# Optimization experiments

Hardware: AMD Instinct MI355X
Metric: run time of the kernel (lower is better)

Reference implementation:

```python
import jax, jax.numpy as jnp
import numpy as np

N = 50000      # nodes
E = 400000     # edges (before self-loops)
IN = 128       # in_channels
OUT = 64       # out_channels (per-head; concat=False averages heads)
HEADS = 8      # heads of first GAT layer; second layer has 1 head
NEG_SLOPE = 0.2


def _glorot(key, shape, fan_in, fan_out):
    s = jnp.sqrt(2.0 / (fan_in + fan_out)).astype(jnp.float32)
    return jax.random.normal(key, shape, jnp.float32) * s


def setup_inputs() -> dict:
    key = jax.random.key(0)
    ks = jax.random.split(key, 10)
    x = jax.random.normal(ks[0], (N, IN), jnp.float32)
    edge_index = jax.random.randint(ks[1], (2, E), 0, N)
    # layer 1: heads=HEADS, per-head dim OUT
    W1 = _glorot(ks[2], (IN, HEADS * OUT), IN, HEADS * OUT)
    att_src1 = _glorot(ks[3], (HEADS, OUT), OUT, 1)
    att_dst1 = _glorot(ks[4], (HEADS, OUT), OUT, 1)
    b1 = jnp.zeros((OUT,), jnp.float32)
    # layer 2: heads=1
    W2 = _glorot(ks[5], (OUT, 1 * OUT), OUT, OUT)
    att_src2 = _glorot(ks[6], (1, OUT), OUT, 1)
    att_dst2 = _glorot(ks[7], (1, OUT), OUT, 1)
    b2 = jnp.zeros((OUT,), jnp.float32)
    return dict(x=x, edge_index=edge_index, W1=W1, att_src1=att_src1,
                att_dst1=att_dst1, b1=b1, W2=W2, att_src2=att_src2,
                att_dst2=att_dst2, b2=b2)


def gat_conv(x, edge_index, W, att_src, att_dst, bias, heads, ch):
    """PyG GATConv with concat=False (mean over heads), add_self_loops=True."""
    n = x.shape[0]
    loop = jnp.arange(n, dtype=edge_index.dtype)
    src = jnp.concatenate([edge_index[0], loop])  # [E+N]
    dst = jnp.concatenate([edge_index[1], loop])
    h = (x @ W).reshape(n, heads, ch)                     # [N, H, C]
    a_s = jnp.sum(h * att_src, axis=-1)                   # [N, H]
    a_d = jnp.sum(h * att_dst, axis=-1)                   # [N, H]
    e = jax.nn.leaky_relu(a_s[src] + a_d[dst], NEG_SLOPE)  # [E+N, H]
    # numerically stable segment softmax over incoming edges of each dst node
    emax = jax.lax.stop_gradient(
        jax.ops.segment_max(e, dst, num_segments=n))       # [N, H]
    ee = jnp.exp(e - emax[dst])
    denom = jax.ops.segment_sum(ee, dst, num_segments=n)  # [N, H]
    alpha = ee / denom[dst]                                # [E+N, H]
    out = jax.ops.segment_sum(alpha[:, :, None] * h[src], dst,
                              num_segments=n)              # [N, H, C]
    return out.mean(axis=1) + bias                         # [N, C]


def reference(x, edge_index, W1, att_src1, att_dst1, b1,
              W2, att_src2, att_dst2, b2):
    h = gat_conv(x, edge_index, W1, att_src1, att_dst1, b1, HEADS, OUT)
    h = jax.nn.elu(h)
    return gat_conv(h, edge_index, W2, att_src2, att_dst2, b2, 1, OUT)
```

## Files before the change

kernel.cpp:

```cpp
#include <hip/hip_runtime.h>
#include <cstdint>
#include <cstddef>

#define NEG_SLOPE 0.2f

typedef short bf16x8 __attribute__((ext_vector_type(8)));
typedef float f32x4 __attribute__((ext_vector_type(4)));
typedef float f32x2 __attribute__((ext_vector_type(2)));

__device__ __forceinline__ unsigned short f2bf(float f) {
  unsigned u = __float_as_uint(f);
  u = u + 0x7FFFu + ((u >> 16) & 1u);
  return (unsigned short)(u >> 16);
}
__device__ __forceinline__ float bf2f(unsigned short b) {
  return __uint_as_float((unsigned)b << 16);
}
__device__ __forceinline__ f32x2 unpk(unsigned xv) {
  f32x2 r;
  r.x = __uint_as_float(xv << 16);
  r.y = __uint_as_float(xv & 0xFFFF0000u);
  return r;
}
__device__ __forceinline__ float rlf(float v, int l) {
  return __uint_as_float(
      (unsigned)__builtin_amdgcn_readlane((int)__float_as_uint(v), l));
}

__global__ __launch_bounds__(256) void prep_all(
    const int* __restrict__ ei, int* __restrict__ counts,
    int* __restrict__ posb,
    const float* __restrict__ x, unsigned short* __restrict__ xb,
    const float* __restrict__ W1, const float* __restrict__ att_s1,
    const float* __restrict__ att_d1, unsigned short* __restrict__ AsAdT,
    unsigned short* __restrict__ WbT,
    const float* __restrict__ W2, unsigned short* __restrict__ W2t,
    const float* __restrict__ att_s2, const float* __restrict__ att_d2,
    float* __restrict__ AsAd2,
    int E, int ET, int N, int B0, int B1) {
  int b = blockIdx.x, tid = threadIdx.x;
  if (b < B0) {
    int i = b * 256 + tid;
    if (i < ET) {
      int dst = (i < E) ? ei[E + i] : (i - E);
      int pos = atomicAdd(&counts[dst], 1);
      posb[i] = pos;
    }
    return;
  }
  b -= B0;
  if (b < B1) {
    int i = b * 256 + tid;
    if (i < N * 32) {
      float4 v = ((const float4*)x)[i];
      ushort4 o;
      o.x = f2bf(v.x); o.y = f2bf(v.y); o.z = f2bf(v.z); o.w = f2bf(v.w);
      ((ushort4*)xb)[i] = o;
    }
    return;
  }
  b -= B1;
  if (b < 8) {
    int i = b * 256 + tid;
    int o = i >> 7, k = i & 127, h = o & 7;
    const float* att = (o < 8) ? att_s1 : att_d1;
    float s = 0.f;
    for (int c = 0; c < 64; c++) s += W1[(size_t)k * 512 + h * 64 + c] * att[h * 64 + c];
    AsAdT[i] = f2bf(s);
    return;
  }
  b -= 8;
  if (b < 256) {
    int i = b * 256 + tid;
    int o = i >> 10, k = i & 1023, h = k >> 7, c = k & 127;
    WbT[i] = f2bf(W1[(size_t)c * 512 + h * 64 + o]);
    return;
  }
  b -= 256;
  if (b < 16) {
    int i = b * 256 + tid;
    if (i < 64 * 64) {
      int k = i >> 6, nn = i & 63;
      W2t[(size_t)nn * 64 + k] = f2bf(W2[i]);
    }
    return;
  }
  {
    int i = tid;
    if (i < 128) {
      int o = i >> 6, k = i & 63;
      const float* att = (o == 0) ? att_s2 : att_d2;
      float s = 0.f;
      for (int c = 0; c < 64; c++) s += W2[(size_t)k * 64 + c] * att[c];
      AsAd2[i] = s;
    }
  }
}

__global__ __launch_bounds__(1024) void scan_dots(
    const int* __restrict__ counts, int* __restrict__ offsets,
    const unsigned short* __restrict__ xb, const unsigned short* __restrict__ AsAdT,
    float* __restrict__ asd, int n) {
  if (blockIdx.x == 0) {
    __shared__ int sums[1024];
    int t = threadIdx.x;
    int chunk = (n + 1023) >> 10;
    int start = t * chunk;
    int end = min(start + chunk, n);
    int s = 0;
    for (int i = start; i < end; i++) s += counts[i];
    sums[t] = s;
    __syncthreads();
    for (int off = 1; off < 1024; off <<= 1) {
      int v = (t >= off) ? sums[t - off] : 0;
      __syncthreads();
      sums[t] += v;
      __syncthreads();
    }
    int run = sums[t] - s;
    for (int i = start; i < end; i++) { offsets[i] = run; run += counts[i]; }
    if (t == 1023) offsets[n] = sums[1023];
    return;
  }
  int tid = threadIdx.x;
  int wave = tid >> 6, lane = tid & 63;
  int q = lane >> 4, t = lane & 15;
  int row0 = (blockIdx.x - 1) * 256 + wave * 16;
  int arow = row0 + t; if (arow > n - 1) arow = n - 1;
  const bf16x8* aptr = (const bf16x8*)(xb + (size_t)arow * 128);
  const bf16x8* bptr = (const bf16x8*)(AsAdT + t * 128);
  f32x4 acc = (f32x4){0.f, 0.f, 0.f, 0.f};
  #pragma unroll
  for (int s = 0; s < 4; s++)
    acc = __builtin_amdgcn_mfma_f32_16x16x32_bf16(aptr[s * 4 + q], bptr[s * 4 + q],
                                                  acc, 0, 0, 0);
  #pragma unroll
  for (int r = 0; r < 4; r++) {
    int row = row0 + q * 4 + r;
    if (row < n) asd[row * 16 + t] = acc[r];
  }
}

__global__ __launch_bounds__(256) void fill_csr(
    const int* __restrict__ ei, const int* __restrict__ offsets,
    const int* __restrict__ posb, int* __restrict__ srcs, int E, int ET) {
  int i = blockIdx.x * 256 + threadIdx.x;
  if (i >= ET) return;
  int src, dst;
  if (i < E) { src = ei[i]; dst = ei[E + i]; } else { src = dst = i - E; }
  srcs[offsets[dst] + posb[i]] = src;
}

#define CONSUME8R(RV, W, ACC)                                         \
  _Pragma("unroll")                                                   \
  for (int k = 0; k < 8; k++) {                                       \
    f32x2 x2 = unpk(RV[k]);                                           \
    ACC[0] += x2 * rlf(W, k * 8 + 0);                                 \
    ACC[1] += x2 * rlf(W, k * 8 + 1);                                 \
    ACC[2] += x2 * rlf(W, k * 8 + 2);                                 \
    ACC[3] += x2 * rlf(W, k * 8 + 3);                                 \
    ACC[4] += x2 * rlf(W, k * 8 + 4);                                 \
    ACC[5] += x2 * rlf(W, k * 8 + 5);                                 \
    ACC[6] += x2 * rlf(W, k * 8 + 6);                                 \
    ACC[7] += x2 * rlf(W, k * 8 + 7);                                 \
  }

__global__ __launch_bounds__(512, 8) void agg1_gemm(
    const int* __restrict__ offsets, const int* __restrict__ srcs,
    const float* __restrict__ asd, const unsigned short* __restrict__ xb,
    const unsigned short* __restrict__ WbT, const float* __restrict__ b1,
    const float* __restrict__ AsAd2, unsigned short* __restrict__ zb,
    float* __restrict__ as2, float* __restrict__ ad2, int N) {
  __shared__ unsigned short sh[8 * 1032];
  int tid = threadIdx.x;
  int wv = tid >> 6, lane = tid & 63;
  int nb = blockIdx.x;
  {
    int node = nb * 8 + wv;
    f32x2 acc[8];
    #pragma unroll
    for (int h = 0; h < 8; h++) acc[h] = (f32x2){0.f, 0.f};
    float wsl = 0.f;
    int beg = offsets[node], end = offsets[node + 1];
    int jl = end - 1;
    float adv = asd[(size_t)node * 16 + 8 + (lane & 7)];
    for (int cb = beg; cb < end; cb += 16) {
      int cnt = min(16, end - cb);
      int sAll = srcs[min(cb + (lane & 15), jl)];
      int swa = srcs[min(cb + (lane >> 3), jl)];
      float asva = asd[(size_t)(unsigned)swa * 16 + (lane & 7)];
      float asvb = 0.f;
      if (cnt > 8) {
        int swb = srcs[min(cb + 8 + (lane >> 3), jl)];
        asvb = asd[(size_t)(unsigned)swb * 16 + (lane & 7)];
      }
      unsigned rva[8] = {0, 0, 0, 0, 0, 0, 0, 0};
      unsigned rvb[8] = {0, 0, 0, 0, 0, 0, 0, 0};
      #pragma unroll
      for (int k = 0; k < 4; k++) {
        int se = __builtin_amdgcn_readlane(sAll, k);
        rva[k] = *(const unsigned*)&xb[(size_t)(unsigned)se * 128 + 2 * lane];
      }
      if (cnt > 4) {
        #pragma unroll
        for (int k = 4; k < 8; k++) {
          int se = __builtin_amdgcn_readlane(sAll, k);
          rva[k] = *(const unsigned*)&xb[(size_t)(unsigned)se * 128 + 2 * lane];
        }
      }
      if (cnt > 8) {
        #pragma unroll
        for (int k = 0; k < 4; k++) {
          int se = __builtin_amdgcn_readlane(sAll, k + 8);
          rvb[k] = *(const unsigned*)&xb[(size_t)(unsigned)se * 128 + 2 * lane];
        }
      }
      if (cnt > 12) {
        #pragma unroll
        for (int k = 4; k < 8; k++) {
          int se = __builtin_amdgcn_readlane(sAll, k + 8);
          rvb[k] = *(const unsigned*)&xb[(size_t)(unsigned)se * 128 + 2 * lane];
        }
      }
      float wa, wb = 0.f;
      {
        float v = asva + adv;
        v = (v > 0.f) ? v : NEG_SLOPE * v;
        wa = (cb + (lane >> 3) < end) ? __expf(v) : 0.f;
      }
      if (cnt > 8) {
        float v = asvb + adv;
        v = (v > 0.f) ? v : NEG_SLOPE * v;
        wb = (cb + 8 + (lane >> 3) < end) ? __expf(v) : 0.f;
      }
      wsl += wa + wb;
      CONSUME8R(rva, wa, acc);
      if (cnt > 8) { CONSUME8R(rvb, wb, acc); }
    }
    wsl += __shfl_xor(wsl, 8, 64);
    wsl += __shfl_xor(wsl, 16, 64);
    wsl += __shfl_xor(wsl, 32, 64);
    #pragma unroll
    for (int h = 0; h < 8; h++) {
      float tot = rlf(wsl, h);
      float iv = 0.125f / tot;
      unsigned o = (unsigned)f2bf(acc[h].x * iv) | ((unsigned)f2bf(acc[h].y * iv) << 16);
      *(unsigned*)&sh[wv * 1032 + h * 128 + 2 * lane] = o;
    }
  }
  __syncthreads();
  if (wv < 4) {
    int q = lane >> 4, t = lane & 15;
    f32x4 acc4 = (f32x4){0.f, 0.f, 0.f, 0.f};
    const unsigned short* bbase = WbT + (size_t)(wv * 16 + t) * 1024;
    #pragma unroll 8
    for (int s = 0; s < 32; s++) {
      bf16x8 af = *(const bf16x8*)&sh[(t & 7) * 1032 + s * 32 + q * 8];
      bf16x8 bf = *(const bf16x8*)&bbase[s * 32 + q * 8];
      acc4 = __builtin_amdgcn_mfma_f32_16x16x32_bf16(af, bf, acc4, 0, 0, 0);
    }
    int col = wv * 16 + t;
    float bias = b1[col];
    float vs = AsAd2[col], vd = AsAd2[64 + col];
    #pragma unroll
    for (int r = 0; r < 4; r++) {
      int row = q * 4 + r;
      float v = acc4[r] + bias;
      v = (v > 0.f) ? v : (__expf(v) - 1.f);
      float s = v * vs, d = v * vd;
      #pragma unroll
      for (int off = 1; off < 16; off <<= 1) {
        s += __shfl_xor(s, off, 64);
        d += __shfl_xor(d, off, 64);
      }
      if (row < 8) {
        int node = nb * 8 + row;
        zb[(size_t)node * 64 + col] = f2bf(v);
        if (t == 0) {
          atomicAdd(&as2[node], s);
          atomicAdd(&ad2[node], d);
        }
      }
    }
  }
}

__global__ __launch_bounds__(512, 8) void agg2_gemm(
    const int* __restrict__ offsets, const int* __restrict__ srcs,
    const float* __restrict__ as2, const float* __restrict__ ad2,
    const unsigned short* __restrict__ zb, const unsigned short* __restrict__ W2t,
    const float* __restrict__ b2, float* __restrict__ out, int N) {
  __shared__ unsigned short sh[8 * 72];
  int tid = threadIdx.x;
  int wv = tid >> 6, lane = tid & 63;
  int nb = blockIdx.x;
  {
    int node = nb * 8 + wv;
    int half = lane >> 5;
    float adv = ad2[node];
    int beg = offsets[node], end = offsets[node + 1];
    int jl = end - 1;
    f32x2 acc = (f32x2){0.f, 0.f};
    float wsl = 0.f;
    for (int cb = beg; cb < end; cb += 16) {
      int cnt = min(16, end - cb);
      int sAll = srcs[min(cb + (lane & 15), jl)];
      float asv = as2[sAll];
      unsigned rv[8] = {0, 0, 0, 0, 0, 0, 0, 0};
      #pragma unroll
      for (int k = 0; k < 2; k++) {
        int s0 = __builtin_amdgcn_readlane(sAll, 2 * k);
        int s1 = __builtin_amdgcn_readlane(sAll, 2 * k + 1);
        int se = half ? s1 : s0;
        rv[k] = *(const unsigned*)&zb[(size_t)(unsigned)se * 64 + 2 * (lane & 31)];
      }
      if (cnt > 4) {
        #pragma unroll
        for (int k = 2; k < 4; k++) {
          int s0 = __builtin_amdgcn_readlane(sAll, 2 * k);
          int s1 = __builtin_amdgcn_readlane(sAll, 2 * k + 1);
          int se = half ? s1 : s0;
          rv[k] = *(const unsigned*)&zb[(size_t)(unsigned)se * 64 + 2 * (lane & 31)];
        }
      }
      if (cnt > 8) {
        #pragma unroll
        for (int k = 4; k < 6; k++) {
          int s0 = __builtin_amdgcn_readlane(sAll, 2 * k);
          int s1 = __builtin_amdgcn_readlane(sAll, 2 * k + 1);
          int se = half ? s1 : s0;
          rv[k] = *(const unsigned*)&zb[(size_t)(unsigned)se * 64 + 2 * (lane & 31)];
        }
      }
      if (cnt > 12) {
        #pragma unroll
        for (int k = 6; k < 8; k++) {
          int s0 = __builtin_amdgcn_readlane(sAll, 2 * k);
          int s1 = __builtin_amdgcn_readlane(sAll, 2 * k + 1);
          int se = half ? s1 : s0;
          rv[k] = *(const unsigned*)&zb[(size_t)(unsigned)se * 64 + 2 * (lane & 31)];
        }
      }
      float v = asv + adv;
      v = (v > 0.f) ? v : NEG_SLOPE * v;
      float wl = (cb + (lane & 15) < end) ? __expf(v) : 0.f;
      if (lane < 16) wsl += wl;
      #pragma unroll
      for (int k = 0; k < 4; k++) {
        float w0 = rlf(wl, 2 * k);
        float w1 = rlf(wl, 2 * k + 1);
        float w = half ? w1 : w0;
        acc += unpk(rv[k]) * w;
      }
      if (cnt > 8) {
        #pragma unroll
        for (int k = 4; k < 8; k++) {
          float w0 = rlf(wl, 2 * k);
          float w1 = rlf(wl, 2 * k + 1);
          float w = half ? w1 : w0;
          acc += unpk(rv[k]) * w;
        }
      }
    }
    wsl += __shfl_xor(wsl, 1, 64);
    wsl += __shfl_xor(wsl, 2, 64);
    wsl += __shfl_xor(wsl, 4, 64);
    wsl += __shfl_xor(wsl, 8, 64);
    float tot = rlf(wsl, 0);
    acc.x += __shfl_xor(acc.x, 32, 64);
    acc.y += __shfl_xor(acc.y, 32, 64);
    if (lane < 32) {
      float inv = 1.f / tot;
      unsigned o = (unsigned)f2bf(acc.x * inv) | ((unsigned)f2bf(acc.y * inv) << 16);
      *(unsigned*)&sh[wv * 72 + 2 * lane] = o;
    }
  }
  __syncthreads();
  if (wv < 4) {
    int q = lane >> 4, t = lane & 15;
    f32x4 acc4 = (f32x4){0.f, 0.f, 0.f, 0.f};
    const unsigned short* bbase = W2t + (size_t)(wv * 16 + t) * 64;
    #pragma unroll
    for (int s = 0; s < 2; s++) {
      bf16x8 af = *(const bf16x8*)&sh[(t & 7) * 72 + s * 32 + q * 8];
      bf16x8 bf = *(const bf16x8*)&bbase[s * 32 + q * 8];
      acc4 = __builtin_amdgcn_mfma_f32_16x16x32_bf16(af, bf, acc4, 0, 0, 0);
    }
    int col = wv * 16 + t;
    float bias = b2[col];
    #pragma unroll
    for (int r = 0; r < 4; r++) {
      int row = q * 4 + r;
      if (row < 8) {
        int node = nb * 8 + row;
        if (node < N) out[(size_t)node * 64 + col] = acc4[r] + bias;
      }
    }
  }
}

extern "C" void kernel_launch(void* const* d_in, const int* in_sizes, int n_in,
                              void* d_out, int out_size, void* d_ws, size_t ws_size,
                              hipStream_t stream) {
  const int IN = 128;
  const int N = in_sizes[0] / IN;
  const int E = in_sizes[1] / 2;
  const int ET = E + N;

  const float* x        = (const float*)d_in[0];
  const int*   ei       = (const int*)d_in[1];
  const float* W1       = (const float*)d_in[2];
  const float* att_src1 = (const float*)d_in[3];
  const float* att_dst1 = (const float*)d_in[4];
  const float* b1       = (const float*)d_in[5];
  const float* W2       = (const float*)d_in[6];
  const float* att_src2 = (const float*)d_in[7];
  const float* att_dst2 = (const float*)d_in[8];
  const float* b2       = (const float*)d_in[9];
  float* out = (float*)d_out;

  char* base = (char*)d_ws;
  size_t off = 0;
  auto alloc = [&](size_t bytes) -> char* {
    char* p = base + off;
    off = (off + bytes + 255) & ~(size_t)255;
    return p;
  };
  unsigned short* xb    = (unsigned short*)alloc((size_t)N * 128 * 2);
  unsigned short* AsAdT = (unsigned short*)alloc((size_t)16 * 128 * 2);
  unsigned short* WbT   = (unsigned short*)alloc((size_t)64 * 1024 * 2);
  unsigned short* W2t   = (unsigned short*)alloc((size_t)64 * 64 * 2);
  unsigned short* zb    = (unsigned short*)alloc((size_t)N * 64 * 2);
  float* AsAd2 = (float*)alloc((size_t)128 * 4);
  float* asd1  = (float*)alloc((size_t)N * 16 * 4);
  int* offsets = (int*)alloc((size_t)(N + 1) * 4);
  int* srcs    = (int*)alloc((size_t)ET * 4);
  int* posb    = (int*)alloc((size_t)ET * 4);
  char* zero_begin = base + off;
  int* counts  = (int*)alloc((size_t)N * 4);
  float* a_s2  = (float*)alloc((size_t)N * 4);
  float* a_d2  = (float*)alloc((size_t)N * 4);
  char* zero_end = base + off;

  hipMemsetAsync(zero_begin, 0, (size_t)(zero_end - zero_begin), stream);

  const int TB = 256;
  auto cdiv = [](int a, int b) { return (a + b - 1) / b; };

  int B0 = cdiv(ET, TB);
  int B1 = cdiv(N * 32, TB);
  prep_all<<<B0 + B1 + 8 + 256 + 16 + 1, TB, 0, stream>>>(
      ei, counts, posb, x, xb, W1, att_src1, att_dst1, AsAdT, WbT, W2, W2t,
      att_src2, att_dst2, AsAd2, E, ET, N, B0, B1);

  scan_dots<<<1 + cdiv(N, 256), 1024, 0, stream>>>(counts, offsets, xb, AsAdT,
                                                   asd1, N);

  fill_csr<<<cdiv(ET, TB), TB, 0, stream>>>(ei, offsets, posb, srcs, E, ET);

  agg1_gemm<<<cdiv(N, 8), 512, 0, stream>>>(offsets, srcs, asd1, xb, WbT, b1,
                                            AsAd2, zb, a_s2, a_d2, N);

  agg2_gemm<<<cdiv(N, 8), 512, 0, stream>>>(offsets, srcs, a_s2, a_d2, zb,
                                            W2t, b2, out, N);
}
```

Before: 338.8 us.

## Process 16 nodes per block to fill MFMA rows and skip partial edge groups

Blocks of the two aggregation+GEMM kernels grow from 8 to 16 waves, so each handles 16 destination nodes. The MFMA tile's 16 rows are now all real nodes instead of half being duplicates, which halves the number of blocks and the per-node weight loads. The consume loops are also split into 4-edge chunks so partially filled 16-edge groups skip the unused multiply-adds. Larger 1024-thread blocks with a launch-bounds hint of 8 blocks per CU may squeeze register budgets or reduce occupancy flexibility, and the N<16-multiple boundary is no longer guarded in agg1.

```diff
diff --git a/kernel.cpp b/kernel.cpp
--- a/kernel.cpp
+++ b/kernel.cpp
@@ -151,32 +151,32 @@
   srcs[offsets[dst] + posb[i]] = src;
 }
 
-#define CONSUME8R(RV, W, ACC)                                         \
+#define CONSUME4R(RV, K0, W, ACC)                                     \
   _Pragma("unroll")                                                   \
-  for (int k = 0; k < 8; k++) {                                       \
+  for (int k = K0; k < K0 + 4; k++) {                                 \
     f32x2 x2 = unpk(RV[k]);                                           \
-    ACC[0] += x2 * rlf(W, k * 8 + 0);                                 \
-    ACC[1] += x2 * rlf(W, k * 8 + 1);                                 \
-    ACC[2] += x2 * rlf(W, k * 8 + 2);                                 \
-    ACC[3] += x2 * rlf(W, k * 8 + 3);                                 \
-    ACC[4] += x2 * rlf(W, k * 8 + 4);                                 \
-    ACC[5] += x2 * rlf(W, k * 8 + 5);                                 \
-    ACC[6] += x2 * rlf(W, k * 8 + 6);                                 \
-    ACC[7] += x2 * rlf(W, k * 8 + 7);                                 \
-  }
-
-__global__ __launch_bounds__(512, 8) void agg1_gemm(
+    ACC[0] += x2 * rlf(W, (k & 7) * 8 + 0);                           \
+    ACC[1] += x2 * rlf(W, (k & 7) * 8 + 1);                           \
+    ACC[2] += x2 * rlf(W, (k & 7) * 8 + 2);                           \
+    ACC[3] += x2 * rlf(W, (k & 7) * 8 + 3);                           \
+    ACC[4] += x2 * rlf(W, (k & 7) * 8 + 4);                           \
+    ACC[5] += x2 * rlf(W, (k & 7) * 8 + 5);                           \
+    ACC[6] += x2 * rlf(W, (k & 7) * 8 + 6);                           \
+    ACC[7] += x2 * rlf(W, (k & 7) * 8 + 7);                           \
+  }
+
+__global__ __launch_bounds__(1024, 8) void agg1_gemm(
     const int* __restrict__ offsets, const int* __restrict__ srcs,
     const float* __restrict__ asd, const unsigned short* __restrict__ xb,
     const unsigned short* __restrict__ WbT, const float* __restrict__ b1,
     const float* __restrict__ AsAd2, unsigned short* __restrict__ zb,
     float* __restrict__ as2, float* __restrict__ ad2, int N) {
-  __shared__ unsigned short sh[8 * 1032];
+  __shared__ unsigned short sh[16 * 1032];
   int tid = threadIdx.x;
   int wv = tid >> 6, lane = tid & 63;
   int nb = blockIdx.x;
   {
-    int node = nb * 8 + wv;
+    int node = nb * 16 + wv;
     f32x2 acc[8];
     #pragma unroll
     for (int h = 0; h < 8; h++) acc[h] = (f32x2){0.f, 0.f};
@@ -194,8 +194,7 @@
         int swb = srcs[min(cb + 8 + (lane >> 3), jl)];
         asvb = asd[(size_t)(unsigned)swb * 16 + (lane & 7)];
       }
-      unsigned rva[8] = {0, 0, 0, 0, 0, 0, 0, 0};
-      unsigned rvb[8] = {0, 0, 0, 0, 0, 0, 0, 0};
+      unsigned rva[8], rvb[8];
       #pragma unroll
       for (int k = 0; k < 4; k++) {
         int se = __builtin_amdgcn_readlane(sAll, k);
@@ -234,8 +233,10 @@
         wb = (cb + 8 + (lane >> 3) < end) ? __expf(v) : 0.f;
       }
       wsl += wa + wb;
-      CONSUME8R(rva, wa, acc);
-      if (cnt > 8) { CONSUME8R(rvb, wb, acc); }
+      CONSUME4R(rva, 0, wa, acc);
+      if (cnt > 4) { CONSUME4R(rva, 4, wa, acc); }
+      if (cnt > 8) { CONSUME4R(rvb, 0, wb, acc); }
+      if (cnt > 12) { CONSUME4R(rvb, 4, wb, acc); }
     }
     wsl += __shfl_xor(wsl, 8, 64);
     wsl += __shfl_xor(wsl, 16, 64);
@@ -255,7 +256,7 @@
     const unsigned short* bbase = WbT + (size_t)(wv * 16 + t) * 1024;
     #pragma unroll 8
     for (int s = 0; s < 32; s++) {
-      bf16x8 af = *(const bf16x8*)&sh[(t & 7) * 1032 + s * 32 + q * 8];
+      bf16x8 af = *(const bf16x8*)&sh[t * 1032 + s * 32 + q * 8];
       bf16x8 bf = *(const bf16x8*)&bbase[s * 32 + q * 8];
       acc4 = __builtin_amdgcn_mfma_f32_16x16x32_bf16(af, bf, acc4, 0, 0, 0);
     }
@@ -265,37 +266,35 @@
     #pragma unroll
     for (int r = 0; r < 4; r++) {
       int row = q * 4 + r;
+      int node = nb * 16 + row;
       float v = acc4[r] + bias;
       v = (v > 0.f) ? v : (__expf(v) - 1.f);
+      zb[(size_t)node * 64 + col] = f2bf(v);
       float s = v * vs, d = v * vd;
       #pragma unroll
       for (int off = 1; off < 16; off <<= 1) {
         s += __shfl_xor(s, off, 64);
         d += __shfl_xor(d, off, 64);
       }
-      if (row < 8) {
-        int node = nb * 8 + row;
-        zb[(size_t)node * 64 + col] = f2bf(v);
-        if (t == 0) {
-          atomicAdd(&as2[node], s);
-          atomicAdd(&ad2[node], d);
-        }
-      }
-    }
-  }
-}
-
-__global__ __launch_bounds__(512, 8) void agg2_gemm(
+      if (t == 0) {
+        atomicAdd(&as2[node], s);
+        atomicAdd(&ad2[node], d);
+      }
+    }
+  }
+}
+
+__global__ __launch_bounds__(1024, 8) void agg2_gemm(
     const int* __restrict__ offsets, const int* __restrict__ srcs,
     const float* __restrict__ as2, const float* __restrict__ ad2,
     const unsigned short* __restrict__ zb, const unsigned short* __restrict__ W2t,
     const float* __restrict__ b2, float* __restrict__ out, int N) {
-  __shared__ unsigned short sh[8 * 72];
+  __shared__ unsigned short sh[16 * 72];
   int tid = threadIdx.x;
   int wv = tid >> 6, lane = tid & 63;
   int nb = blockIdx.x;
   {
-    int node = nb * 8 + wv;
+    int node = nb * 16 + wv;
     int half = lane >> 5;
     float adv = ad2[node];
     int beg = offsets[node], end = offsets[node + 1];
@@ -306,7 +305,7 @@
       int cnt = min(16, end - cb);
       int sAll = srcs[min(cb + (lane & 15), jl)];
       float asv = as2[sAll];
-      unsigned rv[8] = {0, 0, 0, 0, 0, 0, 0, 0};
+      unsigned rv[8];
       #pragma unroll
       for (int k = 0; k < 2; k++) {
         int s0 = __builtin_amdgcn_readlane(sAll, 2 * k);
@@ -346,15 +345,33 @@
       float wl = (cb + (lane & 15) < end) ? __expf(v) : 0.f;
       if (lane < 16) wsl += wl;
       #pragma unroll
-      for (int k = 0; k < 4; k++) {
+      for (int k = 0; k < 2; k++) {
         float w0 = rlf(wl, 2 * k);
         float w1 = rlf(wl, 2 * k + 1);
         float w = half ? w1 : w0;
         acc += unpk(rv[k]) * w;
       }
+      if (cnt > 4) {
+        #pragma unroll
+        for (int k = 2; k < 4; k++) {
+          float w0 = rlf(wl, 2 * k);
+          float w1 = rlf(wl, 2 * k + 1);
+          float w = half ? w1 : w0;
+          acc += unpk(rv[k]) * w;
+        }
+      }
       if (cnt > 8) {
         #pragma unroll
-        for (int k = 4; k < 8; k++) {
+        for (int k = 4; k < 6; k++) {
+          float w0 = rlf(wl, 2 * k);
+          float w1 = rlf(wl, 2 * k + 1);
+          float w = half ? w1 : w0;
+          acc += unpk(rv[k]) * w;
+        }
+      }
+      if (cnt > 12) {
+        #pragma unroll
+        for (int k = 6; k < 8; k++) {
           float w0 = rlf(wl, 2 * k);
           float w1 = rlf(wl, 2 * k + 1);
           float w = half ? w1 : w0;
@@ -382,7 +399,7 @@
     const unsigned short* bbase = W2t + (size_t)(wv * 16 + t) * 64;
     #pragma unroll
     for (int s = 0; s < 2; s++) {
-      bf16x8 af = *(const bf16x8*)&sh[(t & 7) * 72 + s * 32 + q * 8];
+      bf16x8 af = *(const bf16x8*)&sh[t * 72 + s * 32 + q * 8];
       bf16x8 bf = *(const bf16x8*)&bbase[s * 32 + q * 8];
       acc4 = __builtin_amdgcn_mfma_f32_16x16x32_bf16(af, bf, acc4, 0, 0, 0);
     }
@@ -390,11 +407,8 @@
     float bias = b2[col];
     #pragma unroll
     for (int r = 0; r < 4; r++) {
-      int row = q * 4 + r;
-      if (row < 8) {
-        int node = nb * 8 + row;
-        if (node < N) out[(size_t)node * 64 + col] = acc4[r] + bias;
-      }
+      int node = nb * 16 + q * 4 + r;
+      if (node < N) out[(size_t)node * 64 + col] = acc4[r] + bias;
     }
   }
 }
@@ -458,9 +472,9 @@
 
   fill_csr<<<cdiv(ET, TB), TB, 0, stream>>>(ei, offsets, posb, srcs, E, ET);
 
-  agg1_gemm<<<cdiv(N, 8), 512, 0, stream>>>(offsets, srcs, asd1, xb, WbT, b1,
-                                            AsAd2, zb, a_s2, a_d2, N);
-
-  agg2_gemm<<<cdiv(N, 8), 512, 0, stream>>>(offsets, srcs, a_s2, a_d2, zb,
-                                            W2t, b2, out, N);
-}
+  agg1_gemm<<<cdiv(N, 16), 1024, 0, stream>>>(offsets, srcs, asd1, xb, WbT, b1,
+                                              AsAd2, zb, a_s2, a_d2, N);
+
+  agg2_gemm<<<cdiv(N, 16), 1024, 0, stream>>>(offsets, srcs, a_s2, a_d2, zb,
+                                              W2t, b2, out, N);
+}
```

Result: faster. 303.1 us (-10.5%).
